# Performance work log

Hardware: AMD Instinct MI355X
Metric: run time of the kernel (lower is better)

Reference implementation:

```python
import jax, jax.numpy as jnp
import numpy as np

N_NODES = 40000
N_EDGES = 640000
D_FEAT = 128
HIDDEN = 128
N_GRAPHS = 512


def setup_inputs() -> dict:
    key = jax.random.key(0)
    ks = jax.random.split(key, 6)
    x = jax.random.normal(ks[0], (N_NODES, D_FEAT), dtype=jnp.float32)
    edge_index = jax.random.randint(ks[1], (2, N_EDGES), 0, N_NODES, dtype=jnp.int32)
    batch = jnp.sort(jax.random.randint(ks[2], (N_NODES,), 0, N_GRAPHS, dtype=jnp.int32))
    s1 = 1.0 / np.sqrt(D_FEAT)
    s2 = 1.0 / np.sqrt(HIDDEN)
    W1 = jax.random.normal(ks[3], (D_FEAT, HIDDEN), dtype=jnp.float32) * s1
    b1 = jnp.zeros((HIDDEN,), dtype=jnp.float32)
    W2 = jax.random.normal(ks[4], (HIDDEN, HIDDEN), dtype=jnp.float32) * s2
    b2 = jnp.zeros((HIDDEN,), dtype=jnp.float32)
    Wfc = jax.random.normal(ks[5], (HIDDEN, 1), dtype=jnp.float32) * s2
    bfc = jnp.zeros((1,), dtype=jnp.float32)
    return {"x": x, "edge_index": edge_index, "batch": batch,
            "W1": W1, "b1": b1, "W2": W2, "b2": b2, "Wfc": Wfc, "bfc": bfc}


def _gcn_conv(x, edge_index, W, b):
    # PyG GCNConv: linear transform, add self-loops, symmetric deg^{-1/2} norm,
    # scatter-add messages from row (source) to col (target), then bias.
    n = x.shape[0]
    h = x @ W  # [N, H]
    row, col = edge_index[0], edge_index[1]
    ones = jnp.ones_like(col, dtype=h.dtype)
    deg = 1.0 + jax.ops.segment_sum(ones, col, num_segments=n)  # self-loop included
    dinv = jax.lax.rsqrt(deg)  # [N]
    norm = dinv[row] * dinv[col]  # [E]
    msg = h[row] * norm[:, None]  # [E, H]
    out = jax.ops.segment_sum(msg, col, num_segments=n)
    out = out + h * (dinv * dinv)[:, None]  # self-loop contribution
    return out + b


def _mean_pool(x, batch, num_graphs):
    sums = jax.ops.segment_sum(x, batch, num_segments=num_graphs)
    cnt = jax.ops.segment_sum(jnp.ones((x.shape[0],), dtype=x.dtype), batch, num_segments=num_graphs)
    return sums / jnp.maximum(cnt, 1.0)[:, None]


def reference(x, edge_index, batch, W1, b1, W2, b2, Wfc, bfc):
    h = jax.nn.relu(_gcn_conv(x, edge_index, W1, b1))
    h = jax.nn.relu(_gcn_conv(h, edge_index, W2, b2))
    g = _mean_pool(h, batch, N_GRAPHS)  # [G, H]
    return g @ Wfc + bfc  # [G, 1]
```

## Files before the change

kernel.cpp:

```cpp
#include <hip/hip_runtime.h>
#include <hip/hip_fp16.h>

#define N_NODES 40000
#define N_EDGES 640000
#define NFEAT   128
#define N_GRAPHS 512
#define SCAN_NB 157
#define NBKT    157
#define BKT_CAP 8192
#define BIN_BLK_EDGES 2048
#define NBLK_A ((N_EDGES + BIN_BLK_EDGES - 1) / BIN_BLK_EDGES)
#define EPAD_MAX (N_EDGES + 3 * N_NODES)

__global__ void init_misc_kernel(int* __restrict__ gcursor, int* __restrict__ gcnt,
                                 float* __restrict__ out, const float* __restrict__ bfc,
                                 __half* __restrict__ hsent) {
    int t = threadIdx.x;
    if (t < NBKT) gcursor[t] = 0;
    float b = bfc[0];
    for (int i = t; i < N_GRAPHS; i += 256) { gcnt[i] = 0; out[i] = b; }
    if (t < NFEAT) hsent[t] = __float2half(0.0f);
}

__global__ void batch_hist_kernel(const int* __restrict__ batch, int* __restrict__ gcnt, int n) {
    int i = blockIdx.x * blockDim.x + threadIdx.x;
    if (i < n) atomicAdd(&gcnt[batch[i]], 1);
}

__global__ __launch_bounds__(256) void bin_kernel(const int* __restrict__ ei,
                                                  int* __restrict__ gcursor,
                                                  unsigned int* __restrict__ binned) {
    __shared__ int lhist[NBKT];
    __shared__ int lbase[NBKT];
    const int t  = threadIdx.x;
    const int e0 = blockIdx.x * BIN_BLK_EDGES;

    if (t < NBKT) lhist[t] = 0;
    __syncthreads();

    #pragma unroll
    for (int i = 0; i < BIN_BLK_EDGES / 256; ++i) {
        int e = e0 + i * 256 + t;
        if (e < N_EDGES) atomicAdd(&lhist[ei[N_EDGES + e] >> 8], 1);
    }
    __syncthreads();

    if (t < NBKT) { lbase[t] = atomicAdd(&gcursor[t], lhist[t]); lhist[t] = 0; }
    __syncthreads();

    #pragma unroll
    for (int i = 0; i < BIN_BLK_EDGES / 256; ++i) {
        int e = e0 + i * 256 + t;
        if (e < N_EDGES) {
            int c = ei[N_EDGES + e];
            int r = ei[e];
            int bkt = c >> 8;
            int slot = atomicAdd(&lhist[bkt], 1);
            binned[(size_t)bkt * BKT_CAP + lbase[bkt] + slot] =
                (unsigned int)r | ((unsigned int)(c & 255) << 16);
        }
    }
}

__global__ __launch_bounds__(256) void bucket_hist_kernel(const unsigned int* __restrict__ binned,
                                                          const int* __restrict__ gcursor,
                                                          float* __restrict__ dinv,
                                                          int* __restrict__ pdeg) {
    __shared__ int chist[256];
    const int b = blockIdx.x, t = threadIdx.x;
    chist[t] = 0;
    __syncthreads();
    const int cnt = gcursor[b];
    const unsigned int* src = binned + (size_t)b * BKT_CAP;
    for (int i = t; i < cnt; i += 256) atomicAdd(&chist[src[i] >> 16], 1);
    __syncthreads();
    int col = b * 256 + t;
    if (col < N_NODES) {
        int d = chist[t];
        dinv[col] = rsqrtf(1.0f + (float)d);
        pdeg[col] = (d + 3) & ~3;
    }
}

__global__ void scan1_kernel(const int* __restrict__ in, int* __restrict__ out,
                             int* __restrict__ bsums, int n) {
    __shared__ int tmp[256];
    int t = threadIdx.x;
    int i = blockIdx.x * 256 + t;
    int v = (i < n) ? in[i] : 0;
    tmp[t] = v;
    __syncthreads();
    for (int off = 1; off < 256; off <<= 1) {
        int add = (t >= off) ? tmp[t - off] : 0;
        __syncthreads();
        tmp[t] += add;
        __syncthreads();
    }
    if (i < n) out[i] = tmp[t] - v;
    if (t == 255) bsums[blockIdx.x] = tmp[255];
}

__global__ void scan2_kernel(int* __restrict__ bsums, int nb) {
    __shared__ int tmp[256];
    int t = threadIdx.x;
    int v = (t < nb) ? bsums[t] : 0;
    tmp[t] = v;
    __syncthreads();
    for (int off = 1; off < 256; off <<= 1) {
        int add = (t >= off) ? tmp[t - off] : 0;
        __syncthreads();
        tmp[t] += add;
        __syncthreads();
    }
    if (t < nb) bsums[t] = tmp[t] - v;
}

__global__ void scan3_kernel(int* __restrict__ rowptr, const int* __restrict__ bsums,
                             const int* __restrict__ pdeg, int n) {
    int i = blockIdx.x * 256 + threadIdx.x;
    if (i < n) {
        int v = rowptr[i] + bsums[blockIdx.x];
        rowptr[i] = v;
        if (i == n - 1) rowptr[n] = v + pdeg[i];
    }
}

template <typename IdxT>
__global__ __launch_bounds__(256) void bucket_scatter_kernel(const unsigned int* __restrict__ binned,
                                                             const int* __restrict__ gcursor,
                                                             const int* __restrict__ rowptr,
                                                             IdxT* __restrict__ csr) {
    __shared__ int ccur[256];
    const int b = blockIdx.x, t = threadIdx.x;
    int col = b * 256 + t;
    ccur[t] = (col < N_NODES) ? rowptr[col] : 0;
    __syncthreads();
    const int cnt = gcursor[b];
    const unsigned int* src = binned + (size_t)b * BKT_CAP;
    for (int i = t; i < cnt; i += 256) {
        unsigned int u = src[i];
        int slot = atomicAdd(&ccur[u >> 16], 1);
        csr[slot] = (IdxT)(u & 0xFFFFu);
    }
    __syncthreads();
    if (col < N_NODES) {
        int end = rowptr[col + 1];
        for (int p = ccur[t]; p < end; ++p) csr[p] = (IdxT)N_NODES;
    }
}

template <typename OutT>
__global__ __launch_bounds__(256, 4) void gemm64_kernel(const float* __restrict__ X,
                                                        const float* __restrict__ W,
                                                        const float* __restrict__ dinv,
                                                        OutT* __restrict__ H) {
    __shared__ float Ws[128 * 64];
    const int colhalf = blockIdx.x & 1;
    const int tile    = blockIdx.x >> 1;

    for (int i = threadIdx.x; i < 2048; i += 256) {
        int k   = i >> 4;
        int cc4 = (i & 15) * 4;
        *(float4*)(Ws + k * 64 + cc4) = *(const float4*)(W + k * 128 + colhalf * 64 + cc4);
    }
    __syncthreads();

    const int rg = threadIdx.x >> 4;
    const int cg = threadIdx.x & 15;
    const int row0 = tile * 64 + rg * 4;
    const float* x0 = X + (size_t)row0 * NFEAT;

    float acc[4][4] = {};
    float4 xc[4], xn[4];
    #pragma unroll
    for (int i = 0; i < 4; i++) xc[i] = *(const float4*)(x0 + (size_t)i * NFEAT);

    #pragma unroll 4
    for (int k = 0; k < 128; k += 4) {
        const int kn = (k + 4) & 127;
        #pragma unroll
        for (int i = 0; i < 4; i++) xn[i] = *(const float4*)(x0 + (size_t)i * NFEAT + kn);

        float4 wv[4];
        #pragma unroll
        for (int m = 0; m < 4; m++) wv[m] = *(const float4*)(Ws + (k + m) * 64 + cg * 4);

        #pragma unroll
        for (int i = 0; i < 4; i++) {
            const float xi[4] = {xc[i].x, xc[i].y, xc[i].z, xc[i].w};
            #pragma unroll
            for (int m = 0; m < 4; m++) {
                acc[i][0] += xi[m] * wv[m].x;
                acc[i][1] += xi[m] * wv[m].y;
                acc[i][2] += xi[m] * wv[m].z;
                acc[i][3] += xi[m] * wv[m].w;
            }
        }
        #pragma unroll
        for (int i = 0; i < 4; i++) xc[i] = xn[i];
    }

    #pragma unroll
    for (int i = 0; i < 4; i++) {
        float dr = dinv[row0 + i];
        float v0 = acc[i][0] * dr, v1 = acc[i][1] * dr;
        float v2 = acc[i][2] * dr, v3 = acc[i][3] * dr;
        size_t off = (size_t)(row0 + i) * NFEAT + colhalf * 64 + cg * 4;
        if constexpr (sizeof(OutT) == 2) {
            __half2 p0 = __floats2half2_rn(v0, v1);
            __half2 p1 = __floats2half2_rn(v2, v3);
            uint2 pk;
            pk.x = *(unsigned int*)&p0;
            pk.y = *(unsigned int*)&p1;
            *(uint2*)((__half*)H + off) = pk;
        } else {
            float4 o = {v0, v1, v2, v3};
            *(float4*)((float*)H + off) = o;
        }
    }
}

__device__ inline float4 load_h4(const __half* p) {
    uint2 raw = *(const uint2*)p;
    __half2 h0 = *(__half2*)&raw.x;
    __half2 h1 = *(__half2*)&raw.y;
    float2 f0 = __half22float2(h0);
    float2 f1 = __half22float2(h1);
    return make_float4(f0.x, f0.y, f1.x, f1.y);
}

template <typename IdxT, typename IdxV, bool FUSE_POOL>
__global__ __launch_bounds__(256) void gather_h16_kernel(
        const int* __restrict__ rowptr, const IdxT* __restrict__ csr,
        const float* __restrict__ dinv, const __half* __restrict__ Ht,
        const float* __restrict__ bias, float* __restrict__ out,
        const float* __restrict__ Wfc, float* __restrict__ nodedot, int n) {
    int gid  = blockIdx.x * blockDim.x + threadIdx.x;
    int node = gid >> 6;
    if (node >= n) return;
    int lane = threadIdx.x & 63;
    int half = lane >> 5;
    int f4   = (lane & 31) * 4;

    int start = rowptr[node];
    int end   = rowptr[node + 1];

    float4 a0 = {0.f, 0.f, 0.f, 0.f};
    float4 a1 = {0.f, 0.f, 0.f, 0.f};
    if (half == 0) a0 = load_h4(Ht + (size_t)node * NFEAT + f4);

    for (int j = start; j < end; j += 4) {
        IdxV rr = *(const IdxV*)(csr + j);
        int r0 = half ? (int)rr.z : (int)rr.x;
        int r1 = half ? (int)rr.w : (int)rr.y;
        float4 v0 = load_h4(Ht + (size_t)r0 * NFEAT + f4);
        float4 v1 = load_h4(Ht + (size_t)r1 * NFEAT + f4);
        a0.x += v0.x; a0.y += v0.y; a0.z += v0.z; a0.w += v0.w;
        a1.x += v1.x; a1.y += v1.y; a1.z += v1.z; a1.w += v1.w;
    }
    a0.x += a1.x; a0.y += a1.y; a0.z += a1.z; a0.w += a1.w;

    a0.x += __shfl_xor(a0.x, 32, 64);
    a0.y += __shfl_xor(a0.y, 32, 64);
    a0.z += __shfl_xor(a0.z, 32, 64);
    a0.w += __shfl_xor(a0.w, 32, 64);

    if (half == 0) {
        float di  = dinv[node];
        float4 bb = *(const float4*)(bias + f4);
        float4 o;
        o.x = fmaxf(a0.x * di + bb.x, 0.0f);
        o.y = fmaxf(a0.y * di + bb.y, 0.0f);
        o.z = fmaxf(a0.z * di + bb.z, 0.0f);
        o.w = fmaxf(a0.w * di + bb.w, 0.0f);
        if (!FUSE_POOL) {
            *(float4*)(out + (size_t)node * NFEAT + f4) = o;
        } else {
            float4 wf = *(const float4*)(Wfc + f4);
            float d = o.x * wf.x + o.y * wf.y + o.z * wf.z + o.w * wf.w;
            d += __shfl_xor(d, 1, 64);
            d += __shfl_xor(d, 2, 64);
            d += __shfl_xor(d, 4, 64);
            d += __shfl_xor(d, 8, 64);
            d += __shfl_xor(d, 16, 64);
            if (lane == 0) nodedot[node] = d;
        }
    }
}

__global__ void pool_final_kernel(const float* __restrict__ nodedot,
                                  const int* __restrict__ batch,
                                  const int* __restrict__ gcnt,
                                  float* __restrict__ out, int n) {
    int i = blockIdx.x * blockDim.x + threadIdx.x;
    if (i < n) {
        int g = batch[i];
        int c = gcnt[g];
        float cf = (float)(c > 0 ? c : 1);
        atomicAdd(&out[g], nodedot[i] / cf);
    }
}

__global__ void edge_deg_int_kernel(const int* __restrict__ ei, int* __restrict__ degcnt, int E) {
    int e = blockIdx.x * blockDim.x + threadIdx.x;
    if (e < E) atomicAdd(&degcnt[ei[E + e]], 1);
}

__global__ void dinv_from_int_kernel(const int* __restrict__ degcnt, float* __restrict__ dinv, int n) {
    int i = blockIdx.x * blockDim.x + threadIdx.x;
    if (i < n) dinv[i] = rsqrtf(1.0f + (float)degcnt[i]);
}

__global__ __launch_bounds__(256) void edge_scatter_kernel(const int* __restrict__ ei,
                                                           const float* __restrict__ dinv,
                                                           const float* __restrict__ H,
                                                           float* __restrict__ agg,
                                                           int E) {
    long long gid = (long long)blockIdx.x * blockDim.x + threadIdx.x;
    int e = (int)(gid >> 5);
    if (e >= E) return;
    int c4 = ((int)gid & 31) * 4;
    int r = ei[e];
    int c = ei[E + e];
    float norm = dinv[c];
    const float4 hv = *(const float4*)(H + (size_t)r * NFEAT + c4);
    float* dst = agg + (size_t)c * NFEAT + c4;
    atomicAdd(dst + 0, hv.x * norm);
    atomicAdd(dst + 1, hv.y * norm);
    atomicAdd(dst + 2, hv.z * norm);
    atomicAdd(dst + 3, hv.w * norm);
}

__global__ void post_kernel(float* __restrict__ agg, const float* __restrict__ H,
                            const float* __restrict__ dinv, const float* __restrict__ b,
                            int n) {
    int gid = blockIdx.x * blockDim.x + threadIdx.x;
    if (gid >= n * 32) return;
    int node = gid >> 5;
    int c4 = (gid & 31) * 4;
    float s = dinv[node];
    float4 a  = *(float4*)(agg + (size_t)gid * 4);
    float4 hv = *(const float4*)(H + (size_t)gid * 4);
    float4 bb = *(const float4*)(b + c4);
    float4 o;
    o.x = fmaxf(a.x + hv.x * s + bb.x, 0.0f);
    o.y = fmaxf(a.y + hv.y * s + bb.y, 0.0f);
    o.z = fmaxf(a.z + hv.z * s + bb.z, 0.0f);
    o.w = fmaxf(a.w + hv.w * s + bb.w, 0.0f);
    *(float4*)(agg + (size_t)gid * 4) = o;
}

__global__ __launch_bounds__(128) void pool_fc_kernel(const float* __restrict__ H,
                                                      const int* __restrict__ batch,
                                                      const float* __restrict__ Wfc,
                                                      const float* __restrict__ bfc,
                                                      float* __restrict__ out, int n) {
    int g = blockIdx.x;
    int tid = threadIdx.x;
    int lo = 0, hi = n;
    while (lo < hi) { int mid = (lo + hi) >> 1; if (batch[mid] < g) lo = mid + 1; else hi = mid; }
    int start = lo;
    hi = n;
    while (lo < hi) { int mid = (lo + hi) >> 1; if (batch[mid] < g + 1) lo = mid + 1; else hi = mid; }
    int end = lo;

    float acc = 0.0f;
    for (int nd = start; nd < end; ++nd) acc += H[(size_t)nd * NFEAT + tid];
    float cnt = (float)((end - start) > 0 ? (end - start) : 1);
    float v = (acc / cnt) * Wfc[tid];

    __shared__ float red[128];
    red[tid] = v;
    __syncthreads();
    #pragma unroll
    for (int s = 64; s > 0; s >>= 1) {
        if (tid < s) red[tid] += red[tid + s];
        __syncthreads();
    }
    if (tid == 0) out[g] = red[0] + bfc[0];
}

template <typename IdxT, typename IdxV>
static void run_csr_path(const float* x, const int* ei, const int* batch,
                         const float* W1, const float* b1, const float* W2,
                         const float* b2, const float* Wfc, const float* bfc,
                         float* out, void* d_ws, hipStream_t stream) {
    char* ws = (char*)d_ws;
    const size_t hbytes = (size_t)(N_NODES + 1) * NFEAT * sizeof(__half);
    const size_t obytes = (size_t)N_NODES * NFEAT * sizeof(float);
    __half* hbuf  = (__half*)ws;
    float*  obuf  = (float*)(ws + hbytes);
    IdxT*   csr   = (IdxT*)(ws + hbytes + obytes);
    char*   p     = ws + hbytes + obytes + ((size_t)EPAD_MAX * sizeof(IdxT) + 15) / 16 * 16;
    int*    rowptr = (int*)p;                p += ((size_t)(N_NODES + 1) * 4 + 15) / 16 * 16;
    float*  dinv   = (float*)p;              p += ((size_t)N_NODES * 4 + 15) / 16 * 16;
    int*    gcnt   = (int*)p;

    unsigned int* binned = (unsigned int*)obuf;
    int* pdeg    = (int*)obuf + NBKT * BKT_CAP;
    int* bsums   = pdeg + N_NODES;
    int* gcursor = bsums + SCAN_NB;
    float* nodedot = (float*)obuf;

    init_misc_kernel<<<1, 256, 0, stream>>>(gcursor, gcnt, out, bfc,
                                            hbuf + (size_t)N_NODES * NFEAT);
    batch_hist_kernel<<<SCAN_NB, 256, 0, stream>>>(batch, gcnt, N_NODES);
    bin_kernel<<<NBLK_A, 256, 0, stream>>>(ei, gcursor, binned);
    bucket_hist_kernel<<<NBKT, 256, 0, stream>>>(binned, gcursor, dinv, pdeg);
    scan1_kernel<<<SCAN_NB, 256, 0, stream>>>(pdeg, rowptr, bsums, N_NODES);
    scan2_kernel<<<1, 256, 0, stream>>>(bsums, SCAN_NB);
    scan3_kernel<<<SCAN_NB, 256, 0, stream>>>(rowptr, bsums, pdeg, N_NODES);
    bucket_scatter_kernel<IdxT><<<NBKT, 256, 0, stream>>>(binned, gcursor, rowptr, csr);

    gemm64_kernel<__half><<<(N_NODES / 64) * 2, 256, 0, stream>>>(x, W1, dinv, hbuf);
    gather_h16_kernel<IdxT, IdxV, false><<<(N_NODES * 64) / 256, 256, 0, stream>>>(
        rowptr, csr, dinv, hbuf, b1, obuf, nullptr, nullptr, N_NODES);

    gemm64_kernel<__half><<<(N_NODES / 64) * 2, 256, 0, stream>>>(obuf, W2, dinv, hbuf);
    gather_h16_kernel<IdxT, IdxV, true><<<(N_NODES * 64) / 256, 256, 0, stream>>>(
        rowptr, csr, dinv, hbuf, b2, nullptr, Wfc, nodedot, N_NODES);

    pool_final_kernel<<<SCAN_NB, 256, 0, stream>>>(nodedot, batch, gcnt, out, N_NODES);
}

extern "C" void kernel_launch(void* const* d_in, const int* in_sizes, int n_in,
                              void* d_out, int out_size, void* d_ws, size_t ws_size,
                              hipStream_t stream) {
    const float* x     = (const float*)d_in[0];
    const int*   ei    = (const int*)  d_in[1];
    const int*   batch = (const int*)  d_in[2];
    const float* W1    = (const float*)d_in[3];
    const float* b1    = (const float*)d_in[4];
    const float* W2    = (const float*)d_in[5];
    const float* b2    = (const float*)d_in[6];
    const float* Wfc   = (const float*)d_in[7];
    const float* bfc   = (const float*)d_in[8];
    float* out = (float*)d_out;

    const size_t hbytes = (size_t)(N_NODES + 1) * NFEAT * sizeof(__half);
    const size_t obytes = (size_t)N_NODES * NFEAT * sizeof(float);
    const size_t tail   = ((size_t)(N_NODES + 1) * 4 + 15) / 16 * 16
                        + ((size_t)N_NODES * 4 + 15) / 16 * 16
                        + (size_t)N_GRAPHS * 4;
    const size_t needA = hbytes + obytes + ((size_t)EPAD_MAX * 4 + 15) / 16 * 16 + tail;
    const size_t needB = hbytes + obytes + ((size_t)EPAD_MAX * 2 + 15) / 16 * 16 + tail;

    if (ws_size >= needA) {
        run_csr_path<int, int4>(x, ei, batch, W1, b1, W2, b2, Wfc, bfc, out, d_ws, stream);
    } else if (ws_size >= needB) {
        run_csr_path<unsigned short, ushort4>(x, ei, batch, W1, b1, W2, b2, Wfc, bfc, out, d_ws, stream);
    } else {
        float* ws   = (float*)d_ws;
        int*   degc = (int*)ws;
        float* dinv = ws + N_NODES;
        float* hbuf = ws + 2 * N_NODES;
        float* agg  = hbuf + (size_t)N_NODES * NFEAT;
        const size_t fb2 = (size_t)N_NODES * NFEAT * sizeof(float);

        hipMemsetAsync(degc, 0, (size_t)N_NODES * sizeof(int), stream);
        edge_deg_int_kernel<<<N_EDGES / 256, 256, 0, stream>>>(ei, degc, N_EDGES);
        dinv_from_int_kernel<<<SCAN_NB, 256, 0, stream>>>(degc, dinv, N_NODES);

        hipMemsetAsync(agg, 0, fb2, stream);
        gemm64_kernel<float><<<(N_NODES / 64) * 2, 256, 0, stream>>>(x, W1, dinv, hbuf);
        edge_scatter_kernel<<<(N_EDGES * 32) / 256, 256, 0, stream>>>(ei, dinv, hbuf, agg, N_EDGES);
        post_kernel<<<(N_NODES * 32) / 256, 256, 0, stream>>>(agg, hbuf, dinv, b1, N_NODES);

        gemm64_kernel<float><<<(N_NODES / 64) * 2, 256, 0, stream>>>(agg, W2, dinv, hbuf);
        hipMemsetAsync(agg, 0, fb2, stream);
        edge_scatter_kernel<<<(N_EDGES * 32) / 256, 256, 0, stream>>>(ei, dinv, hbuf, agg, N_EDGES);
        post_kernel<<<(N_NODES * 32) / 256, 256, 0, stream>>>(agg, hbuf, dinv, b2, N_NODES);

        pool_fc_kernel<<<N_GRAPHS, 128, 0, stream>>>(agg, batch, Wfc, bfc, out, N_NODES);
    }
}
```

Baseline: 285.8 us.

## Fuse scan stages, store layer-1 output in fp16, widen GEMM tile, fuse pooling

Several changes are made together. The per-bucket degree scan moves into bucket_hist, which cuts the three-kernel scan down to one small scan kernel plus a base offset applied in bucket_scatter. bin_kernel keeps destination indices in registers so they are not reloaded, and the GEMM now computes 128 rows per tile with half-precision input for layer 2. The intermediate activations are stored as fp16 instead of fp32, the gather loop is unrolled to eight edges with four accumulators, and mean pooling is folded into the second gather through atomics. The goal is fewer launches and less memory traffic, in exchange for extra fp16 rounding and more register pressure in the GEMM.

```diff
diff --git a/kernel.cpp b/kernel.cpp
--- a/kernel.cpp
+++ b/kernel.cpp
@@ -11,6 +11,7 @@
 #define BIN_BLK_EDGES 2048
 #define NBLK_A ((N_EDGES + BIN_BLK_EDGES - 1) / BIN_BLK_EDGES)
 #define EPAD_MAX (N_EDGES + 3 * N_NODES)
+#define GEMM_TILES ((N_NODES + 127) / 128)
 
 __global__ void init_misc_kernel(int* __restrict__ gcursor, int* __restrict__ gcnt,
                                  float* __restrict__ out, const float* __restrict__ bfc,
@@ -38,10 +39,12 @@
     if (t < NBKT) lhist[t] = 0;
     __syncthreads();
 
+    int creg[BIN_BLK_EDGES / 256];
     #pragma unroll
     for (int i = 0; i < BIN_BLK_EDGES / 256; ++i) {
         int e = e0 + i * 256 + t;
-        if (e < N_EDGES) atomicAdd(&lhist[ei[N_EDGES + e] >> 8], 1);
+        creg[i] = (e < N_EDGES) ? ei[N_EDGES + e] : -1;
+        if (creg[i] >= 0) atomicAdd(&lhist[creg[i] >> 8], 1);
     }
     __syncthreads();
 
@@ -50,9 +53,9 @@
 
     #pragma unroll
     for (int i = 0; i < BIN_BLK_EDGES / 256; ++i) {
-        int e = e0 + i * 256 + t;
-        if (e < N_EDGES) {
-            int c = ei[N_EDGES + e];
+        int c = creg[i];
+        if (c >= 0) {
+            int e = e0 + i * 256 + t;
             int r = ei[e];
             int bkt = c >> 8;
             int slot = atomicAdd(&lhist[bkt], 1);
@@ -65,8 +68,10 @@
 __global__ __launch_bounds__(256) void bucket_hist_kernel(const unsigned int* __restrict__ binned,
                                                           const int* __restrict__ gcursor,
                                                           float* __restrict__ dinv,
-                                                          int* __restrict__ pdeg) {
+                                                          int* __restrict__ rowptr,
+                                                          int* __restrict__ bsums) {
     __shared__ int chist[256];
+    __shared__ int scn[256];
     const int b = blockIdx.x, t = threadIdx.x;
     chist[t] = 0;
     __syncthreads();
@@ -74,20 +79,27 @@
     const unsigned int* src = binned + (size_t)b * BKT_CAP;
     for (int i = t; i < cnt; i += 256) atomicAdd(&chist[src[i] >> 16], 1);
     __syncthreads();
-    int col = b * 256 + t;
-    if (col < N_NODES) {
-        int d = chist[t];
-        dinv[col] = rsqrtf(1.0f + (float)d);
-        pdeg[col] = (d + 3) & ~3;
-    }
-}
-
-__global__ void scan1_kernel(const int* __restrict__ in, int* __restrict__ out,
-                             int* __restrict__ bsums, int n) {
+    const int col = b * 256 + t;
+    const int valid = (col < N_NODES);
+    int d = chist[t];
+    if (valid) dinv[col] = rsqrtf(1.0f + (float)d);
+    int pd = valid ? ((d + 3) & ~3) : 0;
+    scn[t] = pd;
+    __syncthreads();
+    for (int off = 1; off < 256; off <<= 1) {
+        int add = (t >= off) ? scn[t - off] : 0;
+        __syncthreads();
+        scn[t] += add;
+        __syncthreads();
+    }
+    if (valid) rowptr[col] = scn[t] - pd;
+    if (t == 255) bsums[b] = scn[255];
+}
+
+__global__ void scan157_kernel(int* __restrict__ bsums, int* __restrict__ rowptr) {
     __shared__ int tmp[256];
     int t = threadIdx.x;
-    int i = blockIdx.x * 256 + t;
-    int v = (i < n) ? in[i] : 0;
+    int v = (t < NBKT) ? bsums[t] : 0;
     tmp[t] = v;
     __syncthreads();
     for (int off = 1; off < 256; off <<= 1) {
@@ -96,44 +108,26 @@
         tmp[t] += add;
         __syncthreads();
     }
-    if (i < n) out[i] = tmp[t] - v;
-    if (t == 255) bsums[blockIdx.x] = tmp[255];
-}
-
-__global__ void scan2_kernel(int* __restrict__ bsums, int nb) {
-    __shared__ int tmp[256];
-    int t = threadIdx.x;
-    int v = (t < nb) ? bsums[t] : 0;
-    tmp[t] = v;
-    __syncthreads();
-    for (int off = 1; off < 256; off <<= 1) {
-        int add = (t >= off) ? tmp[t - off] : 0;
-        __syncthreads();
-        tmp[t] += add;
-        __syncthreads();
-    }
-    if (t < nb) bsums[t] = tmp[t] - v;
-}
-
-__global__ void scan3_kernel(int* __restrict__ rowptr, const int* __restrict__ bsums,
-                             const int* __restrict__ pdeg, int n) {
-    int i = blockIdx.x * 256 + threadIdx.x;
-    if (i < n) {
-        int v = rowptr[i] + bsums[blockIdx.x];
-        rowptr[i] = v;
-        if (i == n - 1) rowptr[n] = v + pdeg[i];
-    }
+    if (t < NBKT) bsums[t] = tmp[t] - v;
+    if (t == 255) rowptr[N_NODES] = tmp[255];
 }
 
 template <typename IdxT>
 __global__ __launch_bounds__(256) void bucket_scatter_kernel(const unsigned int* __restrict__ binned,
                                                              const int* __restrict__ gcursor,
-                                                             const int* __restrict__ rowptr,
+                                                             const int* __restrict__ bsums,
+                                                             int* __restrict__ rowptr,
                                                              IdxT* __restrict__ csr) {
     __shared__ int ccur[256];
     const int b = blockIdx.x, t = threadIdx.x;
-    int col = b * 256 + t;
-    ccur[t] = (col < N_NODES) ? rowptr[col] : 0;
+    const int col = b * 256 + t;
+    const int base = bsums[b];
+    int startp = 0;
+    if (col < N_NODES) {
+        startp = rowptr[col] + base;
+        rowptr[col] = startp;
+    }
+    ccur[t] = startp;
     __syncthreads();
     const int cnt = gcursor[b];
     const unsigned int* src = binned + (size_t)b * BKT_CAP;
@@ -144,16 +138,29 @@
     }
     __syncthreads();
     if (col < N_NODES) {
-        int end = rowptr[col + 1];
-        for (int p = ccur[t]; p < end; ++p) csr[p] = (IdxT)N_NODES;
-    }
-}
-
-template <typename OutT>
-__global__ __launch_bounds__(256, 4) void gemm64_kernel(const float* __restrict__ X,
-                                                        const float* __restrict__ W,
-                                                        const float* __restrict__ dinv,
-                                                        OutT* __restrict__ H) {
+        int cur = ccur[t];
+        int deg = cur - startp;
+        int endp = startp + ((deg + 3) & ~3);
+        for (int p = cur; p < endp; ++p) csr[p] = (IdxT)N_NODES;
+    }
+}
+
+__device__ inline float4 load_h4(const __half* p) {
+    uint2 raw = *(const uint2*)p;
+    __half2 h0 = *(__half2*)&raw.x;
+    __half2 h1 = *(__half2*)&raw.y;
+    float2 f0 = __half22float2(h0);
+    float2 f1 = __half22float2(h1);
+    return make_float4(f0.x, f0.y, f1.x, f1.y);
+}
+__device__ inline float4 load4v(const float* p)  { return *(const float4*)p; }
+__device__ inline float4 load4v(const __half* p) { return load_h4(p); }
+
+template <typename InT>
+__global__ __launch_bounds__(256, 4) void gemm128x64_kernel(const InT* __restrict__ X,
+                                                            const float* __restrict__ W,
+                                                            const float* __restrict__ dinv,
+                                                            __half* __restrict__ H) {
     __shared__ float Ws[128 * 64];
     const int colhalf = blockIdx.x & 1;
     const int tile    = blockIdx.x >> 1;
@@ -165,29 +172,29 @@
     }
     __syncthreads();
 
-    const int rg = threadIdx.x >> 4;
-    const int cg = threadIdx.x & 15;
-    const int row0 = tile * 64 + rg * 4;
-    const float* x0 = X + (size_t)row0 * NFEAT;
-
-    float acc[4][4] = {};
-    float4 xc[4], xn[4];
+    const int rg  = threadIdx.x >> 4;
+    const int cg4 = (threadIdx.x & 15) * 4;
+    const int row0 = tile * 128 + rg * 8;
+
+    const InT* xp[8];
     #pragma unroll
-    for (int i = 0; i < 4; i++) xc[i] = *(const float4*)(x0 + (size_t)i * NFEAT);
-
-    #pragma unroll 4
+    for (int i = 0; i < 8; i++) {
+        int rr = row0 + i; if (rr > N_NODES - 1) rr = N_NODES - 1;
+        xp[i] = X + (size_t)rr * NFEAT;
+    }
+
+    float acc[8][4] = {};
+    #pragma unroll 2
     for (int k = 0; k < 128; k += 4) {
-        const int kn = (k + 4) & 127;
+        float4 xv[8];
         #pragma unroll
-        for (int i = 0; i < 4; i++) xn[i] = *(const float4*)(x0 + (size_t)i * NFEAT + kn);
-
+        for (int i = 0; i < 8; i++) xv[i] = load4v(xp[i] + k);
         float4 wv[4];
         #pragma unroll
-        for (int m = 0; m < 4; m++) wv[m] = *(const float4*)(Ws + (k + m) * 64 + cg * 4);
-
+        for (int m = 0; m < 4; m++) wv[m] = *(const float4*)(Ws + (k + m) * 64 + cg4);
         #pragma unroll
-        for (int i = 0; i < 4; i++) {
-            const float xi[4] = {xc[i].x, xc[i].y, xc[i].z, xc[i].w};
+        for (int i = 0; i < 8; i++) {
+            const float xi[4] = {xv[i].x, xv[i].y, xv[i].z, xv[i].w};
             #pragma unroll
             for (int m = 0; m < 4; m++) {
                 acc[i][0] += xi[m] * wv[m].x;
@@ -196,45 +203,30 @@
                 acc[i][3] += xi[m] * wv[m].w;
             }
         }
-        #pragma unroll
-        for (int i = 0; i < 4; i++) xc[i] = xn[i];
     }
 
     #pragma unroll
-    for (int i = 0; i < 4; i++) {
-        float dr = dinv[row0 + i];
-        float v0 = acc[i][0] * dr, v1 = acc[i][1] * dr;
-        float v2 = acc[i][2] * dr, v3 = acc[i][3] * dr;
-        size_t off = (size_t)(row0 + i) * NFEAT + colhalf * 64 + cg * 4;
-        if constexpr (sizeof(OutT) == 2) {
-            __half2 p0 = __floats2half2_rn(v0, v1);
-            __half2 p1 = __floats2half2_rn(v2, v3);
+    for (int i = 0; i < 8; i++) {
+        int row = row0 + i;
+        if (row < N_NODES) {
+            float dr = dinv[row];
+            __half2 p0 = __floats2half2_rn(acc[i][0] * dr, acc[i][1] * dr);
+            __half2 p1 = __floats2half2_rn(acc[i][2] * dr, acc[i][3] * dr);
             uint2 pk;
             pk.x = *(unsigned int*)&p0;
             pk.y = *(unsigned int*)&p1;
-            *(uint2*)((__half*)H + off) = pk;
-        } else {
-            float4 o = {v0, v1, v2, v3};
-            *(float4*)((float*)H + off) = o;
+            *(uint2*)(H + (size_t)row * NFEAT + colhalf * 64 + cg4) = pk;
         }
     }
-}
-
-__device__ inline float4 load_h4(const __half* p) {
-    uint2 raw = *(const uint2*)p;
-    __half2 h0 = *(__half2*)&raw.x;
-    __half2 h1 = *(__half2*)&raw.y;
-    float2 f0 = __half22float2(h0);
-    float2 f1 = __half22float2(h1);
-    return make_float4(f0.x, f0.y, f1.x, f1.y);
 }
 
 template <typename IdxT, typename IdxV, bool FUSE_POOL>
 __global__ __launch_bounds__(256) void gather_h16_kernel(
         const int* __restrict__ rowptr, const IdxT* __restrict__ csr,
         const float* __restrict__ dinv, const __half* __restrict__ Ht,
-        const float* __restrict__ bias, float* __restrict__ out,
-        const float* __restrict__ Wfc, float* __restrict__ nodedot, int n) {
+        const float* __restrict__ bias, __half* __restrict__ outh,
+        const float* __restrict__ Wfc, const int* __restrict__ batch,
+        const int* __restrict__ gcnt, float* __restrict__ out, int n) {
     int gid  = blockIdx.x * blockDim.x + threadIdx.x;
     int node = gid >> 6;
     if (node >= n) return;
@@ -247,18 +239,40 @@
 
     float4 a0 = {0.f, 0.f, 0.f, 0.f};
     float4 a1 = {0.f, 0.f, 0.f, 0.f};
+    float4 a2 = {0.f, 0.f, 0.f, 0.f};
+    float4 a3 = {0.f, 0.f, 0.f, 0.f};
     if (half == 0) a0 = load_h4(Ht + (size_t)node * NFEAT + f4);
 
-    for (int j = start; j < end; j += 4) {
-        IdxV rr = *(const IdxV*)(csr + j);
-        int r0 = half ? (int)rr.z : (int)rr.x;
-        int r1 = half ? (int)rr.w : (int)rr.y;
+    int j = start;
+    for (; j + 7 < end; j += 8) {
+        IdxV ra = *(const IdxV*)(csr + j);
+        IdxV rb = *(const IdxV*)(csr + j + 4);
+        int r0 = half ? (int)ra.z : (int)ra.x;
+        int r1 = half ? (int)ra.w : (int)ra.y;
+        int r2 = half ? (int)rb.z : (int)rb.x;
+        int r3 = half ? (int)rb.w : (int)rb.y;
+        float4 v0 = load_h4(Ht + (size_t)r0 * NFEAT + f4);
+        float4 v1 = load_h4(Ht + (size_t)r1 * NFEAT + f4);
+        float4 v2 = load_h4(Ht + (size_t)r2 * NFEAT + f4);
+        float4 v3 = load_h4(Ht + (size_t)r3 * NFEAT + f4);
+        a0.x += v0.x; a0.y += v0.y; a0.z += v0.z; a0.w += v0.w;
+        a1.x += v1.x; a1.y += v1.y; a1.z += v1.z; a1.w += v1.w;
+        a2.x += v2.x; a2.y += v2.y; a2.z += v2.z; a2.w += v2.w;
+        a3.x += v3.x; a3.y += v3.y; a3.z += v3.z; a3.w += v3.w;
+    }
+    if (j < end) {
+        IdxV ra = *(const IdxV*)(csr + j);
+        int r0 = half ? (int)ra.z : (int)ra.x;
+        int r1 = half ? (int)ra.w : (int)ra.y;
         float4 v0 = load_h4(Ht + (size_t)r0 * NFEAT + f4);
         float4 v1 = load_h4(Ht + (size_t)r1 * NFEAT + f4);
         a0.x += v0.x; a0.y += v0.y; a0.z += v0.z; a0.w += v0.w;
         a1.x += v1.x; a1.y += v1.y; a1.z += v1.z; a1.w += v1.w;
     }
-    a0.x += a1.x; a0.y += a1.y; a0.z += a1.z; a0.w += a1.w;
+    a0.x += a1.x + a2.x + a3.x;
+    a0.y += a1.y + a2.y + a3.y;
+    a0.z += a1.z + a2.z + a3.z;
+    a0.w += a1.w + a2.w + a3.w;
 
     a0.x += __shfl_xor(a0.x, 32, 64);
     a0.y += __shfl_xor(a0.y, 32, 64);
@@ -274,7 +288,12 @@
         o.z = fmaxf(a0.z * di + bb.z, 0.0f);
         o.w = fmaxf(a0.w * di + bb.w, 0.0f);
         if (!FUSE_POOL) {
-            *(float4*)(out + (size_t)node * NFEAT + f4) = o;
+            __half2 p0 = __floats2half2_rn(o.x, o.y);
+            __half2 p1 = __floats2half2_rn(o.z, o.w);
+            uint2 pk;
+            pk.x = *(unsigned int*)&p0;
+            pk.y = *(unsigned int*)&p1;
+            *(uint2*)(outh + (size_t)node * NFEAT + f4) = pk;
         } else {
             float4 wf = *(const float4*)(Wfc + f4);
             float d = o.x * wf.x + o.y * wf.y + o.z * wf.z + o.w * wf.w;
@@ -283,21 +302,13 @@
             d += __shfl_xor(d, 4, 64);
             d += __shfl_xor(d, 8, 64);
             d += __shfl_xor(d, 16, 64);
-            if (lane == 0) nodedot[node] = d;
+            if (lane == 0) {
+                int g = batch[node];
+                int c = gcnt[g];
+                float cf = (float)(c > 0 ? c : 1);
+                atomicAdd(&out[g], d / cf);
+            }
         }
-    }
-}
-
-__global__ void pool_final_kernel(const float* __restrict__ nodedot,
-                                  const int* __restrict__ batch,
-                                  const int* __restrict__ gcnt,
-                                  float* __restrict__ out, int n) {
-    int i = blockIdx.x * blockDim.x + threadIdx.x;
-    if (i < n) {
-        int g = batch[i];
-        int c = gcnt[g];
-        float cf = (float)(c > 0 ? c : 1);
-        atomicAdd(&out[g], nodedot[i] / cf);
     }
 }
 
@@ -309,6 +320,52 @@
 __global__ void dinv_from_int_kernel(const int* __restrict__ degcnt, float* __restrict__ dinv, int n) {
     int i = blockIdx.x * blockDim.x + threadIdx.x;
     if (i < n) dinv[i] = rsqrtf(1.0f + (float)degcnt[i]);
+}
+
+__global__ __launch_bounds__(256, 4) void gemm64f_kernel(const float* __restrict__ X,
+                                                         const float* __restrict__ W,
+                                                         const float* __restrict__ dinv,
+                                                         float* __restrict__ H) {
+    __shared__ float Ws[128 * 64];
+    const int colhalf = blockIdx.x & 1;
+    const int tile    = blockIdx.x >> 1;
+    for (int i = threadIdx.x; i < 2048; i += 256) {
+        int k   = i >> 4;
+        int cc4 = (i & 15) * 4;
+        *(float4*)(Ws + k * 64 + cc4) = *(const float4*)(W + k * 128 + colhalf * 64 + cc4);
+    }
+    __syncthreads();
+    const int rg = threadIdx.x >> 4;
+    const int cg = threadIdx.x & 15;
+    const int row0 = tile * 64 + rg * 4;
+    const float* x0 = X + (size_t)row0 * NFEAT;
+    float acc[4][4] = {};
+    #pragma unroll 4
+    for (int k = 0; k < 128; k += 4) {
+        float4 xv[4];
+        float4 wv[4];
+        #pragma unroll
+        for (int i = 0; i < 4; i++) xv[i] = *(const float4*)(x0 + (size_t)i * NFEAT + k);
+        #pragma unroll
+        for (int m = 0; m < 4; m++) wv[m] = *(const float4*)(Ws + (k + m) * 64 + cg * 4);
+        #pragma unroll
+        for (int i = 0; i < 4; i++) {
+            const float xi[4] = {xv[i].x, xv[i].y, xv[i].z, xv[i].w};
+            #pragma unroll
+            for (int m = 0; m < 4; m++) {
+                acc[i][0] += xi[m] * wv[m].x;
+                acc[i][1] += xi[m] * wv[m].y;
+                acc[i][2] += xi[m] * wv[m].z;
+                acc[i][3] += xi[m] * wv[m].w;
+            }
+        }
+    }
+    #pragma unroll
+    for (int i = 0; i < 4; i++) {
+        float dr = dinv[row0 + i];
+        float4 o = {acc[i][0] * dr, acc[i][1] * dr, acc[i][2] * dr, acc[i][3] * dr};
+        *(float4*)(H + (size_t)(row0 + i) * NFEAT + colhalf * 64 + cg * 4) = o;
+    }
 }
 
 __global__ __launch_bounds__(256) void edge_scatter_kernel(const int* __restrict__ ei,
@@ -363,12 +420,10 @@
     hi = n;
     while (lo < hi) { int mid = (lo + hi) >> 1; if (batch[mid] < g + 1) lo = mid + 1; else hi = mid; }
     int end = lo;
-
     float acc = 0.0f;
     for (int nd = start; nd < end; ++nd) acc += H[(size_t)nd * NFEAT + tid];
     float cnt = (float)((end - start) > 0 ? (end - start) : 1);
     float v = (acc / cnt) * Wfc[tid];
-
     __shared__ float red[128];
     red[tid] = v;
     __syncthreads();
@@ -387,9 +442,9 @@
                          float* out, void* d_ws, hipStream_t stream) {
     char* ws = (char*)d_ws;
     const size_t hbytes = (size_t)(N_NODES + 1) * NFEAT * sizeof(__half);
-    const size_t obytes = (size_t)N_NODES * NFEAT * sizeof(float);
+    const size_t obytes = (size_t)N_NODES * NFEAT * sizeof(__half);
     __half* hbuf  = (__half*)ws;
-    float*  obuf  = (float*)(ws + hbytes);
+    __half* obuf  = (__half*)(ws + hbytes);
     IdxT*   csr   = (IdxT*)(ws + hbytes + obytes);
     char*   p     = ws + hbytes + obytes + ((size_t)EPAD_MAX * sizeof(IdxT) + 15) / 16 * 16;
     int*    rowptr = (int*)p;                p += ((size_t)(N_NODES + 1) * 4 + 15) / 16 * 16;
@@ -397,30 +452,24 @@
     int*    gcnt   = (int*)p;
 
     unsigned int* binned = (unsigned int*)obuf;
-    int* pdeg    = (int*)obuf + NBKT * BKT_CAP;
-    int* bsums   = pdeg + N_NODES;
-    int* gcursor = bsums + SCAN_NB;
-    float* nodedot = (float*)obuf;
+    int* bsums   = (int*)obuf + NBKT * BKT_CAP;
+    int* gcursor = bsums + NBKT;
 
     init_misc_kernel<<<1, 256, 0, stream>>>(gcursor, gcnt, out, bfc,
                                             hbuf + (size_t)N_NODES * NFEAT);
     batch_hist_kernel<<<SCAN_NB, 256, 0, stream>>>(batch, gcnt, N_NODES);
     bin_kernel<<<NBLK_A, 256, 0, stream>>>(ei, gcursor, binned);
-    bucket_hist_kernel<<<NBKT, 256, 0, stream>>>(binned, gcursor, dinv, pdeg);
-    scan1_kernel<<<SCAN_NB, 256, 0, stream>>>(pdeg, rowptr, bsums, N_NODES);
-    scan2_kernel<<<1, 256, 0, stream>>>(bsums, SCAN_NB);
-    scan3_kernel<<<SCAN_NB, 256, 0, stream>>>(rowptr, bsums, pdeg, N_NODES);
-    bucket_scatter_kernel<IdxT><<<NBKT, 256, 0, stream>>>(binned, gcursor, rowptr, csr);
-
-    gemm64_kernel<__half><<<(N_NODES / 64) * 2, 256, 0, stream>>>(x, W1, dinv, hbuf);
+    bucket_hist_kernel<<<NBKT, 256, 0, stream>>>(binned, gcursor, dinv, rowptr, bsums);
+    scan157_kernel<<<1, 256, 0, stream>>>(bsums, rowptr);
+    bucket_scatter_kernel<IdxT><<<NBKT, 256, 0, stream>>>(binned, gcursor, bsums, rowptr, csr);
+
+    gemm128x64_kernel<float><<<GEMM_TILES * 2, 256, 0, stream>>>(x, W1, dinv, hbuf);
     gather_h16_kernel<IdxT, IdxV, false><<<(N_NODES * 64) / 256, 256, 0, stream>>>(
-        rowptr, csr, dinv, hbuf, b1, obuf, nullptr, nullptr, N_NODES);
-
-    gemm64_kernel<__half><<<(N_NODES / 64) * 2, 256, 0, stream>>>(obuf, W2, dinv, hbuf);
+        rowptr, csr, dinv, hbuf, b1, obuf, nullptr, nullptr, nullptr, nullptr, N_NODES);
+
+    gemm128x64_kernel<__half><<<GEMM_TILES * 2, 256, 0, stream>>>(obuf, W2, dinv, hbuf);
     gather_h16_kernel<IdxT, IdxV, true><<<(N_NODES * 64) / 256, 256, 0, stream>>>(
-        rowptr, csr, dinv, hbuf, b2, nullptr, Wfc, nodedot, N_NODES);
-
-    pool_final_kernel<<<SCAN_NB, 256, 0, stream>>>(nodedot, batch, gcnt, out, N_NODES);
+        rowptr, csr, dinv, hbuf, b2, nullptr, Wfc, batch, gcnt, out, N_NODES);
 }
 
 extern "C" void kernel_launch(void* const* d_in, const int* in_sizes, int n_in,
@@ -438,7 +487,7 @@
     float* out = (float*)d_out;
 
     const size_t hbytes = (size_t)(N_NODES + 1) * NFEAT * sizeof(__half);
-    const size_t obytes = (size_t)N_NODES * NFEAT * sizeof(float);
+    const size_t obytes = (size_t)N_NODES * NFEAT * sizeof(__half);
     const size_t tail   = ((size_t)(N_NODES + 1) * 4 + 15) / 16 * 16
                         + ((size_t)N_NODES * 4 + 15) / 16 * 16
                         + (size_t)N_GRAPHS * 4;
@@ -462,11 +511,11 @@
         dinv_from_int_kernel<<<SCAN_NB, 256, 0, stream>>>(degc, dinv, N_NODES);
 
         hipMemsetAsync(agg, 0, fb2, stream);
-        gemm64_kernel<float><<<(N_NODES / 64) * 2, 256, 0, stream>>>(x, W1, dinv, hbuf);
+        gemm64f_kernel<<<(N_NODES / 64) * 2, 256, 0, stream>>>(x, W1, dinv, hbuf);
         edge_scatter_kernel<<<(N_EDGES * 32) / 256, 256, 0, stream>>>(ei, dinv, hbuf, agg, N_EDGES);
         post_kernel<<<(N_NODES * 32) / 256, 256, 0, stream>>>(agg, hbuf, dinv, b1, N_NODES);
 
-        gemm64_kernel<float><<<(N_NODES / 64) * 2, 256, 0, stream>>>(agg, W2, dinv, hbuf);
+        gemm64f_kernel<<<(N_NODES / 64) * 2, 256, 0, stream>>>(agg, W2, dinv, hbuf);
         hipMemsetAsync(agg, 0, fb2, stream);
         edge_scatter_kernel<<<(N_EDGES * 32) / 256, 256, 0, stream>>>(ei, dinv, hbuf, agg, N_EDGES);
         post_kernel<<<(N_NODES * 32) / 256, 256, 0, stream>>>(agg, hbuf, dinv, b2, N_NODES);
```

New measurement: 333.7 us. 16.8% more time.
